# Optimization experiments

Measured on AMD Instinct MI355X. Metric: run time of the kernel, lower is better.

Reference implementation:

```python
import jax, jax.numpy as jnp
import numpy as np

B, F, C, NS, P, N = 256, 2048, 16384, 65536, 8, 32
T, W_BU, W_H, P_MARGIN, N_MARGIN = 1.0, 1.0, 10.0, 0.1, 0.1


def setup_inputs() -> dict:
    key = jax.random.key(0)
    ks = jax.random.split(key, 8)
    inputs = jax.random.normal(ks[0], (B, F), jnp.float32)
    targets = jax.random.randint(ks[1], (B,), 0, C)
    # batch global indices: unique (original .item() assumes a single match)
    indexs = jax.random.permutation(ks[2], NS)[:B].astype(jnp.int64) if False else jax.random.permutation(ks[2], jnp.arange(NS))[:B]
    # positive candidates drawn from in-batch indices so they are found in `indexs`
    pos_sel = jax.random.randint(ks[3], (B, P), 0, B)
    ppairs = indexs[pos_sel]
    # negative candidates: arbitrary global indices (mostly not in batch)
    npairs = jax.random.randint(ks[4], (B, N), 0, NS)
    all_label_to_clusterid = jax.random.randint(ks[5], (NS,), 0, C)
    V = jax.random.normal(ks[6], (C, F), jnp.float32)
    V = V / jnp.linalg.norm(V, axis=1, keepdims=True)  # bank rows are L2-normalized by the update rule
    return {"inputs": inputs, "targets": targets, "ppairs": ppairs, "npairs": npairs,
            "indexs": indexs, "all_label_to_clusterid": all_label_to_clusterid, "V": V, "epoch": 1}


def _forward(inputs, targets, ppairs, npairs, indexs, all_label_to_clusterid, V, epoch):
    # Exclusive branch: logits against the memory bank (V treated as constant)
    outputs = (inputs @ V.T) * T  # [B, C]
    logp = jax.nn.log_softmax(outputs, axis=1)
    bu_loss = -jnp.mean(jnp.take_along_axis(logp, targets[:, None], axis=1))

    # ms_loss (use_prior=True, use_table=True)
    ni = inputs / jnp.linalg.norm(inputs, axis=1, keepdims=True)
    sims = ni @ ni.T          # [B, B]
    tsims = ni @ V.T          # [B, C]

    # positives found in the batch: (ppair == indexs).nonzero()
    mp = ppairs[:, :, None] == indexs[None, None, :]        # [B, P, B]
    found_p = jnp.any(mp, axis=2)
    idx_p = jnp.argmax(mp, axis=2)
    psim_b = jnp.take_along_axis(sims, idx_p, axis=1)       # [B, P]
    mask_pb = found_p & (ppairs >= 0)
    # table positive: tsims[i, target] appended if nonzero
    tp = jnp.take_along_axis(tsims, targets[:, None], axis=1)  # [B, 1]
    mask_tp = tp != 0
    psims = jnp.concatenate([psim_b, tp], axis=1)           # [B, P+1]
    pmask = jnp.concatenate([mask_pb, mask_tp], axis=1)

    # negatives found in the batch
    mn = npairs[:, :, None] == indexs[None, None, :]        # [B, N, B]
    found_n = jnp.any(mn, axis=2)
    idx_n = jnp.argmax(mn, axis=2)
    nsim_b = jnp.take_along_axis(sims, idx_n, axis=1)       # [B, N]
    mask_nb = found_n & (npairs >= 0)
    # table negative appended for EVERY npair (indent level in original): tsims[i, clusterid[npair]]
    ncid = all_label_to_clusterid[jnp.clip(npairs, 0, None)]
    tn = jnp.take_along_axis(tsims, ncid, axis=1)           # [B, N]
    mask_tn = (npairs >= 0) & (tn != 0)
    nsims = jnp.concatenate([nsim_b, tn], axis=1)           # [B, 2N]
    nmask = jnp.concatenate([mask_nb, mask_tn], axis=1)

    # thresholds: max(nsims) or -3 (+p_margin); min(psims) or 3 (-n_margin)
    p_thrd = jnp.where(jnp.any(nmask, 1), jnp.max(jnp.where(nmask, nsims, -jnp.inf), 1), -3.0) + P_MARGIN
    n_thrd = jnp.where(jnp.any(pmask, 1), jnp.min(jnp.where(pmask, psims, jnp.inf), 1), 3.0) - N_MARGIN

    hp = pmask & (psims < p_thrd[:, None])
    hn = nmask & (nsims > n_thrd[:, None]) & (nsims < 0.999999)

    hp_sum = jnp.sum(jnp.where(hp, jnp.exp(-2.0 * (psims - 0.5)), 0.0))
    hn_sum = jnp.sum(jnp.where(hn, jnp.exp(50.0 * (nsims - 0.5)), 0.0))
    hp_loss = jnp.where(jnp.any(hp), 0.5 * jnp.log1p(hp_sum), 0.0)
    hn_loss = jnp.where(jnp.any(hn), (1.0 / 50.0) * jnp.log1p(hn_sum), 0.0)
    # original builds hpsims/hnsims with torch.tensor(...), which DETACHES them
    h_loss = jax.lax.stop_gradient(hp_loss + hn_loss)

    loss = W_BU * bu_loss + W_H * h_loss
    return loss, outputs


def reference(inputs, targets, ppairs, npairs, indexs, all_label_to_clusterid, V, epoch):
    return _forward(inputs, targets, ppairs, npairs, indexs, all_label_to_clusterid, V, epoch)
```

## Files before the change

kernel.cpp:

```cpp
#include <hip/hip_runtime.h>
#include <hip/hip_bf16.h>
#include <math.h>

#define B_SZ 256
#define F_SZ 2048
#define C_SZ 16384
#define P_SZ 8
#define N_SZ 32
#define NTILE 256

typedef __bf16 bf16x8 __attribute__((ext_vector_type(8)));
typedef float f32x4 __attribute__((ext_vector_type(4)));
typedef unsigned short us8 __attribute__((ext_vector_type(8)));

typedef __attribute__((address_space(3))) unsigned int lds_u32;
typedef __attribute__((address_space(1))) const unsigned int glb_u32;

#define WAITCNT_VM8   0x0F78
#define WAITCNT_VM0   0x0F70
#define WAITCNT_LGKM0 0xC07F

__device__ __forceinline__ unsigned short f2bf(float x) {
    union { float f; unsigned int u; } v; v.f = x;
    unsigned int r = v.u + 0x7FFFu + ((v.u >> 16) & 1u);
    return (unsigned short)(r >> 16);
}

__device__ __forceinline__ unsigned int pk2bf(float x, float y) {
    union { float f; unsigned int u; } a, b; a.f = x; b.f = y;
    return __builtin_amdgcn_perm(b.u + 0x8000u, a.u + 0x8000u, 0x07060302u);
}

__global__ __launch_bounds__(256) void prep_kernel(const float* __restrict__ inputs,
                                                   unsigned short* __restrict__ Abf,
                                                   float* __restrict__ norms) {
    const int row = blockIdx.x;
    const int tid = threadIdx.x;
    const float* rp = inputs + (size_t)row * F_SZ + tid * 8;
    float4 v0 = *(const float4*)(rp);
    float4 v1 = *(const float4*)(rp + 4);
    us8 o;
    o[0]=f2bf(v0.x); o[1]=f2bf(v0.y); o[2]=f2bf(v0.z); o[3]=f2bf(v0.w);
    o[4]=f2bf(v1.x); o[5]=f2bf(v1.y); o[6]=f2bf(v1.z); o[7]=f2bf(v1.w);
    *(us8*)(Abf + (size_t)row * F_SZ + tid * 8) = o;
    float ss = v0.x*v0.x + v0.y*v0.y + v0.z*v0.z + v0.w*v0.w
             + v1.x*v1.x + v1.y*v1.y + v1.z*v1.z + v1.w*v1.w;
    __shared__ float red[256];
    red[tid] = ss; __syncthreads();
    for (int s = 128; s > 0; s >>= 1) { if (tid < s) red[tid] += red[tid+s]; __syncthreads(); }
    if (tid == 0) norms[row] = sqrtf(red[0]);
}

#define BM 128
#define BN 64
#define BK 64
#define BPAD 72
#define KITERS (F_SZ / BK)

__global__ __launch_bounds__(256, 2) void gemm_kernel(const unsigned short* __restrict__ Abf,
                                                      const float* __restrict__ V,
                                                      float* __restrict__ Cout,
                                                      float* __restrict__ pmax,
                                                      float* __restrict__ psum) {
    __shared__ unsigned short As[3][BM * BK];
    __shared__ unsigned short Bs[2][BN * BPAD];
    __shared__ float sm[BM * 2], ss2[BM * 2];

    const int tid = threadIdx.x;
    const int lane = tid & 63;
    const int wid = tid >> 6;
    const int wm = wid >> 1, wn = wid & 1;
    const int q = lane >> 4, l16 = lane & 15;

    const int bid = blockIdx.x;
    const int mhalf = (bid >> 3) & 1;
    const int slab  = (bid & 7) | ((bid >> 4) << 3);
    const int bm0 = mhalf * BM;
    const int bn0 = slab * BN;

    f32x4 acc[4][2];
    #pragma unroll
    for (int i = 0; i < 4; i++)
        #pragma unroll
        for (int j = 0; j < 2; j++) acc[i][j] = (f32x4){0.f, 0.f, 0.f, 0.f};

    const int arow = tid >> 3;
    const int akc = (tid & 7) ^ (arow & 7);
    const unsigned short* AgBase = Abf + (size_t)(bm0 + arow) * F_SZ + akc * 8;

    const int bcol = tid >> 2, bseg = tid & 3;
    const float* BgBase = V + (size_t)(bn0 + bcol) * F_SZ + bseg * 16;
    const int bsoff = bcol * BPAD + bseg * 16;

    float4 a0, a1, a2, a3;
    float4 c0, c1, c2, c3;

    auto issueA = [&](int ring, int k0) {
        #pragma unroll
        for (int j = 0; j < 4; ++j) {
            __builtin_amdgcn_global_load_lds(
                (glb_u32*)(AgBase + (size_t)j * 32 * F_SZ + k0),
                (lds_u32*)&As[ring][(j * 256 + wid * 64) * 8],
                16, 0, 0);
        }
    };
    auto loadB0 = [&](int k0) {
        a0 = *(const float4*)(BgBase + k0);     a1 = *(const float4*)(BgBase + k0 + 4);
        a2 = *(const float4*)(BgBase + k0 + 8); a3 = *(const float4*)(BgBase + k0 + 12);
    };
    auto loadB1 = [&](int k0) {
        c0 = *(const float4*)(BgBase + k0);     c1 = *(const float4*)(BgBase + k0 + 4);
        c2 = *(const float4*)(BgBase + k0 + 8); c3 = *(const float4*)(BgBase + k0 + 12);
    };
    auto writeB = [&](int buf, int set) {
        float4 x0 = set ? c0 : a0, x1 = set ? c1 : a1, x2 = set ? c2 : a2, x3 = set ? c3 : a3;
        uint4 w0 = { pk2bf(x0.x, x0.y), pk2bf(x0.z, x0.w), pk2bf(x1.x, x1.y), pk2bf(x1.z, x1.w) };
        uint4 w1 = { pk2bf(x2.x, x2.y), pk2bf(x2.z, x2.w), pk2bf(x3.x, x3.y), pk2bf(x3.z, x3.w) };
        *(uint4*)&Bs[buf][bsoff] = w0;
        *(uint4*)&Bs[buf][bsoff + 8] = w1;
    };
    auto compute = [&](int ring, int buf) {
        #pragma unroll
        for (int ks = 0; ks < 2; ++ks) {
            bf16x8 af[4], bfv[2];
            const int kc = ks * 4 + q;
            #pragma unroll
            for (int mi = 0; mi < 4; ++mi) {
                const int row = wm * 64 + mi * 16 + l16;
                af[mi] = *(const bf16x8*)&As[ring][row * 64 + (kc ^ (row & 7)) * 8];
            }
            #pragma unroll
            for (int ni = 0; ni < 2; ++ni) {
                const int col = wn * 32 + ni * 16 + l16;
                bfv[ni] = *(const bf16x8*)&Bs[buf][col * BPAD + ks * 32 + q * 8];
            }
            #pragma unroll
            for (int mi = 0; mi < 4; ++mi)
                #pragma unroll
                for (int ni = 0; ni < 2; ++ni)
                    acc[mi][ni] = __builtin_amdgcn_mfma_f32_16x16x32_bf16(af[mi], bfv[ni], acc[mi][ni], 0, 0, 0);
        }
    };

    issueA(0, 0);
    issueA(1, BK);
    loadB0(0);
    __builtin_amdgcn_s_waitcnt(WAITCNT_VM0);
    writeB(0, 0);
    loadB1(BK);
    __syncthreads();

    int cur = 0;
    #pragma unroll 1
    for (int it2 = 0; it2 < KITERS; it2 += 2) {
        {
            const int it = it2;
            if (it + 2 < KITERS) { loadB0((it + 2) * BK); issueA((cur + 2) % 3, (it + 2) * BK); }
            compute(cur, 0);
            if (it + 2 < KITERS)      __builtin_amdgcn_s_waitcnt(WAITCNT_VM8);
            else if (it + 1 < KITERS) __builtin_amdgcn_s_waitcnt(WAITCNT_VM0);
            if (it + 1 < KITERS) {
                writeB(1, 1);
                __builtin_amdgcn_s_waitcnt(WAITCNT_LGKM0);
                __builtin_amdgcn_s_barrier();
            }
        }
        {
            const int it = it2 + 1;
            if (it + 2 < KITERS) { loadB1((it + 2) * BK); issueA(cur, (it + 2) * BK); }
            compute((cur + 1) % 3, 1);
            if (it + 2 < KITERS)      __builtin_amdgcn_s_waitcnt(WAITCNT_VM8);
            else if (it + 1 < KITERS) __builtin_amdgcn_s_waitcnt(WAITCNT_VM0);
            if (it + 1 < KITERS) {
                writeB(0, 0);
                __builtin_amdgcn_s_waitcnt(WAITCNT_LGKM0);
                __builtin_amdgcn_s_barrier();
            }
        }
        cur = (cur + 2) % 3;
    }

    #pragma unroll
    for (int mi = 0; mi < 4; ++mi) {
        const int r0 = bm0 + wm * 64 + mi * 16 + q * 4;
        #pragma unroll
        for (int ni = 0; ni < 2; ++ni) {
            const int c0g = bn0 + wn * 32 + ni * 16 + l16;
            #pragma unroll
            for (int r = 0; r < 4; ++r)
                Cout[(size_t)(r0 + r) * C_SZ + c0g] = acc[mi][ni][r];
        }
    }

    #pragma unroll
    for (int mi = 0; mi < 4; ++mi) {
        #pragma unroll
        for (int r = 0; r < 4; ++r) {
            float mloc = fmaxf(acc[mi][0][r], acc[mi][1][r]);
            #pragma unroll
            for (int off = 1; off < 16; off <<= 1)
                mloc = fmaxf(mloc, __shfl_xor(mloc, off, 64));
            float sloc = __expf(acc[mi][0][r] - mloc) + __expf(acc[mi][1][r] - mloc);
            #pragma unroll
            for (int off = 1; off < 16; off <<= 1)
                sloc += __shfl_xor(sloc, off, 64);
            if (l16 == 0) {
                const int lrow = wm * 64 + mi * 16 + q * 4 + r;
                sm[lrow * 2 + wn] = mloc;
                ss2[lrow * 2 + wn] = sloc;
            }
        }
    }
    __syncthreads();
    if (tid < BM) {
        float m1 = sm[tid * 2], s1 = ss2[tid * 2];
        float m2 = sm[tid * 2 + 1], s2 = ss2[tid * 2 + 1];
        float nm = fmaxf(m1, m2);
        float s = s1 * __expf(m1 - nm) + s2 * __expf(m2 - nm);
        pmax[(bm0 + tid) * NTILE + slab] = nm;
        psum[(bm0 + tid) * NTILE + slab] = s;
    }
}

__global__ __launch_bounds__(256) void pairs_kernel(
    const float* __restrict__ inputs, const int* __restrict__ targets,
    const int* __restrict__ ppairs, const int* __restrict__ npairs,
    const int* __restrict__ indexs, const int* __restrict__ cluster,
    const float* __restrict__ outputs, const float* __restrict__ norms,
    const float* __restrict__ pmax, const float* __restrict__ psum,
    float* __restrict__ bu_part, float* __restrict__ hp_part,
    float* __restrict__ hn_part, int* __restrict__ flag_part)
{
    const int i = blockIdx.x;
    const int tid = threadIdx.x;
    __shared__ int idxbuf[B_SZ];
    __shared__ int pj[P_SZ];
    __shared__ int nj[N_SZ];
    __shared__ float simp[P_SZ];
    __shared__ float simn[N_SZ];
    __shared__ float tnv[N_SZ];
    __shared__ float s_tp;
    __shared__ float rm[256], rs[256];

    idxbuf[tid] = indexs[tid];
    rm[tid] = pmax[i * NTILE + tid];
    rs[tid] = psum[i * NTILE + tid];
    __syncthreads();
    for (int s = 128; s > 0; s >>= 1) {
        if (tid < s) {
            float a = rm[tid], sa = rs[tid];
            float b = rm[tid + s], sb = rs[tid + s];
            float nn = fmaxf(a, b);
            rs[tid] = sa * __expf(a - nn) + sb * __expf(b - nn);
            rm[tid] = nn;
        }
        __syncthreads();
    }

    const float* row = outputs + (size_t)i * C_SZ;
    const float ni_norm = norms[i];

    if (tid == 0) {
        float logZ = rm[0] + logf(rs[0]);
        bu_part[i] = -(row[targets[i]] - logZ);
    }

    if (tid < P_SZ) {
        int pp = ppairs[i * P_SZ + tid];
        int f = -1;
        if (pp >= 0) for (int j = 0; j < B_SZ; j++) if (idxbuf[j] == pp) { f = j; break; }
        pj[tid] = f;
    } else if (tid < P_SZ + N_SZ) {
        int t = tid - P_SZ;
        int np = npairs[i * N_SZ + t];
        int f = -1;
        if (np >= 0) for (int j = 0; j < B_SZ; j++) if (idxbuf[j] == np) { f = j; break; }
        nj[t] = f;
        int cid = cluster[np < 0 ? 0 : np];
        tnv[t] = row[cid] / ni_norm;
    }
    if (tid == P_SZ + N_SZ) s_tp = row[targets[i]] / ni_norm;
    __syncthreads();

    const int lane = tid & 63, wv = tid >> 6;
    for (int qq = wv; qq < P_SZ + N_SZ; qq += 4) {
        int j = (qq < P_SZ) ? pj[qq] : nj[qq - P_SZ];
        float s = 0.f;
        if (j >= 0) {
            const float* xi = inputs + (size_t)i * F_SZ;
            const float* xj = inputs + (size_t)j * F_SZ;
            float d = 0.f;
            for (int k = lane; k < F_SZ; k += 64) d += xi[k] * xj[k];
            for (int off = 32; off > 0; off >>= 1) d += __shfl_down(d, off);
            s = d / (ni_norm * norms[j]);
        }
        if (lane == 0) { if (qq < P_SZ) simp[qq] = s; else simn[qq - P_SZ] = s; }
    }
    __syncthreads();

    if (tid == 0) {
        float psims[P_SZ + 1]; bool pmask[P_SZ + 1];
        for (int p = 0; p < P_SZ; p++) {
            int pp = ppairs[i * P_SZ + p];
            pmask[p] = (pj[p] >= 0) && (pp >= 0);
            psims[p] = simp[p];
        }
        psims[P_SZ] = s_tp; pmask[P_SZ] = (s_tp != 0.0f);

        float nsims[2 * N_SZ]; bool nmask[2 * N_SZ];
        for (int t = 0; t < N_SZ; t++) {
            int np = npairs[i * N_SZ + t];
            nmask[t] = (nj[t] >= 0) && (np >= 0);
            nsims[t] = simn[t];
            nsims[N_SZ + t] = tnv[t];
            nmask[N_SZ + t] = (np >= 0) && (tnv[t] != 0.0f);
        }
        bool anyp = false, anyn = false;
        float maxn = -INFINITY, minp = INFINITY;
        for (int t = 0; t < 2 * N_SZ; t++) if (nmask[t]) { anyn = true; maxn = fmaxf(maxn, nsims[t]); }
        for (int p = 0; p < P_SZ + 1; p++) if (pmask[p]) { anyp = true; minp = fminf(minp, psims[p]); }
        float p_thrd = (anyn ? maxn : -3.0f) + 0.1f;
        float n_thrd = (anyp ? minp : 3.0f) - 0.1f;
        float hps = 0.f, hns = 0.f; int fl = 0;
        for (int p = 0; p < P_SZ + 1; p++)
            if (pmask[p] && psims[p] < p_thrd) { fl |= 1; hps += expf(-2.0f * (psims[p] - 0.5f)); }
        for (int t = 0; t < 2 * N_SZ; t++)
            if (nmask[t] && nsims[t] > n_thrd && nsims[t] < 0.999999f) { fl |= 2; hns += expf(50.0f * (nsims[t] - 0.5f)); }
        hp_part[i] = hps; hn_part[i] = hns; flag_part[i] = fl;
    }
}

__global__ __launch_bounds__(256) void finalize_kernel(
    const float* __restrict__ bu_part, const float* __restrict__ hp_part,
    const float* __restrict__ hn_part, const int* __restrict__ flag_part,
    float* __restrict__ d_out)
{
    __shared__ float r1[256], r2[256], r3[256];
    __shared__ int rf[256];
    const int tid = threadIdx.x;
    r1[tid] = bu_part[tid]; r2[tid] = hp_part[tid]; r3[tid] = hn_part[tid]; rf[tid] = flag_part[tid];
    __syncthreads();
    for (int s = 128; s > 0; s >>= 1) {
        if (tid < s) { r1[tid] += r1[tid+s]; r2[tid] += r2[tid+s]; r3[tid] += r3[tid+s]; rf[tid] |= rf[tid+s]; }
        __syncthreads();
    }
    if (tid == 0) {
        float bu = r1[0] / (float)B_SZ;
        float hp_loss = (rf[0] & 1) ? 0.5f * log1pf(r2[0]) : 0.0f;
        float hn_loss = (rf[0] & 2) ? (1.0f / 50.0f) * log1pf(r3[0]) : 0.0f;
        d_out[0] = 1.0f * bu + 10.0f * (hp_loss + hn_loss);
    }
}

extern "C" void kernel_launch(void* const* d_in, const int* in_sizes, int n_in,
                              void* d_out, int out_size, void* d_ws, size_t ws_size,
                              hipStream_t stream) {
    const float* inputs  = (const float*)d_in[0];
    const int*   targets = (const int*)d_in[1];
    const int*   ppairs  = (const int*)d_in[2];
    const int*   npairs  = (const int*)d_in[3];
    const int*   indexs  = (const int*)d_in[4];
    const int*   cluster = (const int*)d_in[5];
    const float* V       = (const float*)d_in[6];
    float* out = (float*)d_out;

    char* ws = (char*)d_ws;
    unsigned short* Abf = (unsigned short*)ws;
    float* norms   = (float*)(ws + (size_t)B_SZ * F_SZ * 2);
    float* bu_part = norms + B_SZ;
    float* hp_part = bu_part + B_SZ;
    float* hn_part = hp_part + B_SZ;
    int*   flag_part = (int*)(hn_part + B_SZ);
    float* pmax = (float*)(flag_part + B_SZ);
    float* psum = pmax + (size_t)B_SZ * NTILE;

    prep_kernel<<<B_SZ, 256, 0, stream>>>(inputs, Abf, norms);
    gemm_kernel<<<512, 256, 0, stream>>>(Abf, V, out + 1, pmax, psum);
    pairs_kernel<<<B_SZ, 256, 0, stream>>>(inputs, targets, ppairs, npairs, indexs,
                                           cluster, out + 1, norms, pmax, psum,
                                           bu_part, hp_part, hn_part, flag_part);
    finalize_kernel<<<1, 256, 0, stream>>>(bu_part, hp_part, hn_part, flag_part, out);
}
```

Measured before the change: 301.9 us.

## Stage fp32 V tiles via async global-to-LDS loads and widen GEMM block tile

The GEMM now loads the fp32 memory-bank tiles straight into LDS with global_load_lds, using an XOR-swizzled layout and a 3-stage ring. Conversion to bf16 moves into the compute loop, replacing the register-staged load-convert-store path. Blocks grow to 512 threads with a 128x128 tile, which halves the grid and the number of softmax partial tiles. The cost is twice the LDS traffic for B, since it is stored as fp32, extra conversion ALU work in the inner loop, and lower occupancy at one block per CU.

```diff
diff --git a/kernel.cpp b/kernel.cpp
--- a/kernel.cpp
+++ b/kernel.cpp
@@ -7,7 +7,7 @@
 #define C_SZ 16384
 #define P_SZ 8
 #define N_SZ 32
-#define NTILE 256
+#define NTILE 128
 
 typedef __bf16 bf16x8 __attribute__((ext_vector_type(8)));
 typedef float f32x4 __attribute__((ext_vector_type(4)));
@@ -16,9 +16,8 @@
 typedef __attribute__((address_space(3))) unsigned int lds_u32;
 typedef __attribute__((address_space(1))) const unsigned int glb_u32;
 
-#define WAITCNT_VM8   0x0F78
+#define WAITCNT_VM6   0x0F76
 #define WAITCNT_VM0   0x0F70
-#define WAITCNT_LGKM0 0xC07F
 
 __device__ __forceinline__ unsigned short f2bf(float x) {
     union { float f; unsigned int u; } v; v.f = x;
@@ -52,24 +51,23 @@
 }
 
 #define BM 128
-#define BN 64
+#define BN 128
 #define BK 64
-#define BPAD 72
 #define KITERS (F_SZ / BK)
 
-__global__ __launch_bounds__(256, 2) void gemm_kernel(const unsigned short* __restrict__ Abf,
+__global__ __launch_bounds__(512, 1) void gemm_kernel(const unsigned short* __restrict__ Abf,
                                                       const float* __restrict__ V,
                                                       float* __restrict__ Cout,
                                                       float* __restrict__ pmax,
                                                       float* __restrict__ psum) {
     __shared__ unsigned short As[3][BM * BK];
-    __shared__ unsigned short Bs[2][BN * BPAD];
-    __shared__ float sm[BM * 2], ss2[BM * 2];
+    __shared__ float Bs[3][BN * BK];
+    __shared__ float sm[BM * 4], ss2[BM * 4];
 
     const int tid = threadIdx.x;
     const int lane = tid & 63;
-    const int wid = tid >> 6;
-    const int wm = wid >> 1, wn = wid & 1;
+    const int w = tid >> 6;
+    const int wm = w & 1, wn = w >> 1;
     const int q = lane >> 4, l16 = lane & 15;
 
     const int bid = blockIdx.x;
@@ -84,42 +82,30 @@
         #pragma unroll
         for (int j = 0; j < 2; j++) acc[i][j] = (f32x4){0.f, 0.f, 0.f, 0.f};
 
-    const int arow = tid >> 3;
-    const int akc = (tid & 7) ^ (arow & 7);
-    const unsigned short* AgBase = Abf + (size_t)(bm0 + arow) * F_SZ + akc * 8;
-
-    const int bcol = tid >> 2, bseg = tid & 3;
-    const float* BgBase = V + (size_t)(bn0 + bcol) * F_SZ + bseg * 16;
-    const int bsoff = bcol * BPAD + bseg * 16;
-
-    float4 a0, a1, a2, a3;
-    float4 c0, c1, c2, c3;
-
-    auto issueA = [&](int ring, int k0) {
-        #pragma unroll
-        for (int j = 0; j < 4; ++j) {
-            __builtin_amdgcn_global_load_lds(
-                (glb_u32*)(AgBase + (size_t)j * 32 * F_SZ + k0),
-                (lds_u32*)&As[ring][(j * 256 + wid * 64) * 8],
-                16, 0, 0);
-        }
+    int aS0 = w * 128 + lane;
+    int aS1 = aS0 + 64;
+    const int ar0 = aS0 >> 3, ag0 = (aS0 & 7) ^ (ar0 & 7);
+    const int ar1 = aS1 >> 3, ag1 = (aS1 & 7) ^ (ar1 & 7);
+    const unsigned short* Ag0 = Abf + (size_t)(bm0 + ar0) * F_SZ + ag0 * 8;
+    const unsigned short* Ag1 = Abf + (size_t)(bm0 + ar1) * F_SZ + ag1 * 8;
+
+    int bS[4]; const float* Bg[4];
+    #pragma unroll
+    for (int j = 0; j < 4; ++j) {
+        bS[j] = w * 256 + j * 64 + lane;
+        const int col = bS[j] >> 4, gc = (bS[j] & 15) ^ (col & 15);
+        Bg[j] = V + (size_t)(bn0 + col) * F_SZ + gc * 4;
+    }
+    const int aDst0 = (w * 128) * 8, aDst1 = (w * 128 + 64) * 8;
+
+    auto issue = [&](int ring, int k0) {
+        __builtin_amdgcn_global_load_lds((glb_u32*)(Ag0 + k0), (lds_u32*)&As[ring][aDst0], 16, 0, 0);
+        __builtin_amdgcn_global_load_lds((glb_u32*)(Ag1 + k0), (lds_u32*)&As[ring][aDst1], 16, 0, 0);
+        #pragma unroll
+        for (int j = 0; j < 4; ++j)
+            __builtin_amdgcn_global_load_lds((glb_u32*)(Bg[j] + k0), (lds_u32*)&Bs[ring][(w * 256 + j * 64) * 4], 16, 0, 0);
     };
-    auto loadB0 = [&](int k0) {
-        a0 = *(const float4*)(BgBase + k0);     a1 = *(const float4*)(BgBase + k0 + 4);
-        a2 = *(const float4*)(BgBase + k0 + 8); a3 = *(const float4*)(BgBase + k0 + 12);
-    };
-    auto loadB1 = [&](int k0) {
-        c0 = *(const float4*)(BgBase + k0);     c1 = *(const float4*)(BgBase + k0 + 4);
-        c2 = *(const float4*)(BgBase + k0 + 8); c3 = *(const float4*)(BgBase + k0 + 12);
-    };
-    auto writeB = [&](int buf, int set) {
-        float4 x0 = set ? c0 : a0, x1 = set ? c1 : a1, x2 = set ? c2 : a2, x3 = set ? c3 : a3;
-        uint4 w0 = { pk2bf(x0.x, x0.y), pk2bf(x0.z, x0.w), pk2bf(x1.x, x1.y), pk2bf(x1.z, x1.w) };
-        uint4 w1 = { pk2bf(x2.x, x2.y), pk2bf(x2.z, x2.w), pk2bf(x3.x, x3.y), pk2bf(x3.z, x3.w) };
-        *(uint4*)&Bs[buf][bsoff] = w0;
-        *(uint4*)&Bs[buf][bsoff + 8] = w1;
-    };
-    auto compute = [&](int ring, int buf) {
+    auto compute = [&](int ring) {
         #pragma unroll
         for (int ks = 0; ks < 2; ++ks) {
             bf16x8 af[4], bfv[2];
@@ -127,12 +113,18 @@
             #pragma unroll
             for (int mi = 0; mi < 4; ++mi) {
                 const int row = wm * 64 + mi * 16 + l16;
-                af[mi] = *(const bf16x8*)&As[ring][row * 64 + (kc ^ (row & 7)) * 8];
+                af[mi] = *(const bf16x8*)&As[ring][row * 64 + ((kc ^ (row & 7)) * 8)];
             }
             #pragma unroll
             for (int ni = 0; ni < 2; ++ni) {
                 const int col = wn * 32 + ni * 16 + l16;
-                bfv[ni] = *(const bf16x8*)&Bs[buf][col * BPAD + ks * 32 + q * 8];
+                const int c0 = ks * 8 + q * 2;
+                float4 f0 = *(const float4*)&Bs[ring][col * 64 + ((c0 ^ (col & 15)) * 4)];
+                float4 f1 = *(const float4*)&Bs[ring][col * 64 + (((c0 + 1) ^ (col & 15)) * 4)];
+                union { uint4 u; bf16x8 b; } cv;
+                cv.u = (uint4){ pk2bf(f0.x, f0.y), pk2bf(f0.z, f0.w),
+                                pk2bf(f1.x, f1.y), pk2bf(f1.z, f1.w) };
+                bfv[ni] = cv.b;
             }
             #pragma unroll
             for (int mi = 0; mi < 4; ++mi)
@@ -142,42 +134,21 @@
         }
     };
 
-    issueA(0, 0);
-    issueA(1, BK);
-    loadB0(0);
-    __builtin_amdgcn_s_waitcnt(WAITCNT_VM0);
-    writeB(0, 0);
-    loadB1(BK);
-    __syncthreads();
+    issue(0, 0);
+    issue(1, BK);
+    __builtin_amdgcn_s_waitcnt(WAITCNT_VM6);
+    __builtin_amdgcn_s_barrier();
 
     int cur = 0;
     #pragma unroll 1
-    for (int it2 = 0; it2 < KITERS; it2 += 2) {
-        {
-            const int it = it2;
-            if (it + 2 < KITERS) { loadB0((it + 2) * BK); issueA((cur + 2) % 3, (it + 2) * BK); }
-            compute(cur, 0);
-            if (it + 2 < KITERS)      __builtin_amdgcn_s_waitcnt(WAITCNT_VM8);
-            else if (it + 1 < KITERS) __builtin_amdgcn_s_waitcnt(WAITCNT_VM0);
-            if (it + 1 < KITERS) {
-                writeB(1, 1);
-                __builtin_amdgcn_s_waitcnt(WAITCNT_LGKM0);
-                __builtin_amdgcn_s_barrier();
-            }
-        }
-        {
-            const int it = it2 + 1;
-            if (it + 2 < KITERS) { loadB1((it + 2) * BK); issueA(cur, (it + 2) * BK); }
-            compute((cur + 1) % 3, 1);
-            if (it + 2 < KITERS)      __builtin_amdgcn_s_waitcnt(WAITCNT_VM8);
-            else if (it + 1 < KITERS) __builtin_amdgcn_s_waitcnt(WAITCNT_VM0);
-            if (it + 1 < KITERS) {
-                writeB(0, 0);
-                __builtin_amdgcn_s_waitcnt(WAITCNT_LGKM0);
-                __builtin_amdgcn_s_barrier();
-            }
-        }
-        cur = (cur + 2) % 3;
+    for (int it = 0; it < KITERS; ++it) {
+        const int nxt2 = (cur == 0) ? 2 : cur - 1;
+        if (it + 2 < KITERS) issue(nxt2, (it + 2) * BK);
+        compute(cur);
+        if (it + 2 < KITERS)      __builtin_amdgcn_s_waitcnt(WAITCNT_VM6);
+        else if (it + 1 < KITERS) __builtin_amdgcn_s_waitcnt(WAITCNT_VM0);
+        if (it + 1 < KITERS) __builtin_amdgcn_s_barrier();
+        cur = (cur == 2) ? 0 : cur + 1;
     }
 
     #pragma unroll
@@ -206,18 +177,22 @@
                 sloc += __shfl_xor(sloc, off, 64);
             if (l16 == 0) {
                 const int lrow = wm * 64 + mi * 16 + q * 4 + r;
-                sm[lrow * 2 + wn] = mloc;
-                ss2[lrow * 2 + wn] = sloc;
+                sm[lrow * 4 + wn] = mloc;
+                ss2[lrow * 4 + wn] = sloc;
             }
         }
     }
     __syncthreads();
     if (tid < BM) {
-        float m1 = sm[tid * 2], s1 = ss2[tid * 2];
-        float m2 = sm[tid * 2 + 1], s2 = ss2[tid * 2 + 1];
-        float nm = fmaxf(m1, m2);
-        float s = s1 * __expf(m1 - nm) + s2 * __expf(m2 - nm);
-        pmax[(bm0 + tid) * NTILE + slab] = nm;
+        float m = -INFINITY, s = 0.f;
+        #pragma unroll
+        for (int v = 0; v < 4; ++v) {
+            float m2 = sm[tid * 4 + v], s2 = ss2[tid * 4 + v];
+            float nm = fmaxf(m, m2);
+            s = s * __expf(m - nm) + s2 * __expf(m2 - nm);
+            m = nm;
+        }
+        pmax[(bm0 + tid) * NTILE + slab] = m;
         psum[(bm0 + tid) * NTILE + slab] = s;
     }
 }
@@ -240,13 +215,15 @@
     __shared__ float simn[N_SZ];
     __shared__ float tnv[N_SZ];
     __shared__ float s_tp;
-    __shared__ float rm[256], rs[256];
+    __shared__ float rm[NTILE], rs[NTILE];
 
     idxbuf[tid] = indexs[tid];
-    rm[tid] = pmax[i * NTILE + tid];
-    rs[tid] = psum[i * NTILE + tid];
-    __syncthreads();
-    for (int s = 128; s > 0; s >>= 1) {
+    if (tid < NTILE) {
+        rm[tid] = pmax[i * NTILE + tid];
+        rs[tid] = psum[i * NTILE + tid];
+    }
+    __syncthreads();
+    for (int s = NTILE / 2; s > 0; s >>= 1) {
         if (tid < s) {
             float a = rm[tid], sa = rs[tid];
             float b = rm[tid + s], sb = rs[tid + s];
@@ -375,7 +352,7 @@
     float* psum = pmax + (size_t)B_SZ * NTILE;
 
     prep_kernel<<<B_SZ, 256, 0, stream>>>(inputs, Abf, norms);
-    gemm_kernel<<<512, 256, 0, stream>>>(Abf, V, out + 1, pmax, psum);
+    gemm_kernel<<<256, 512, 0, stream>>>(Abf, V, out + 1, pmax, psum);
     pairs_kernel<<<B_SZ, 256, 0, stream>>>(inputs, targets, ppairs, npairs, indexs,
                                            cluster, out + 1, norms, pmax, psum,
                                            bu_part, hp_part, hn_part, flag_part);
```

After: 308.0 us. 2.0% more time.
